# Optimization experiments

Hardware: AMD Instinct MI355X
Metric: run time of the kernel (lower is better)

The kernel has to match this reference:

```python
import jax, jax.numpy as jnp
import numpy as np

T = 2048      # sequence length (block_size)
C = 4096      # n_embd
H = 32        # n_head
KVH = 8       # n_kv_head
D = 128       # head_dim = n_embd // n_head
NEG_INF = -40000.0
ROPE_BASE = 10000.0


def setup_inputs() -> dict:
    key = jax.random.key(0)
    ks = jax.random.split(key, 5)
    x = jax.random.normal(ks[0], (T, C), jnp.float32)
    # nn.Linear weights stored as (in, out); y = x @ W. Small init for numerical sanity.
    Wq = jax.random.normal(ks[1], (C, H * D), jnp.float32) * 0.02
    Wk = jax.random.normal(ks[2], (C, KVH * D), jnp.float32) * 0.02
    Wv = jax.random.normal(ks[3], (C, KVH * D), jnp.float32) * 0.02
    Wo = jax.random.normal(ks[4], (C, C), jnp.float32) * 0.02
    # Standard LLaMA-style RoPE tables: (T, D)
    inv_freq = 1.0 / (ROPE_BASE ** (np.arange(0, D, 2, dtype=np.float32) / D))
    freqs = np.outer(np.arange(T, dtype=np.float32), inv_freq)  # (T, D/2)
    emb = np.concatenate([freqs, freqs], axis=-1)                # (T, D)
    cos = jnp.asarray(np.cos(emb), jnp.float32)
    sin = jnp.asarray(np.sin(emb), jnp.float32)
    # Additive causal mask (T, T): 0 on/below diagonal, neg_inf above.
    causal = np.tril(np.ones((T, T), dtype=bool))
    mask = jnp.where(jnp.asarray(causal), 0.0, NEG_INF).astype(jnp.float32)
    return {"x": x, "Wq": Wq, "Wk": Wk, "Wv": Wv, "Wo": Wo,
            "cos": cos, "sin": sin, "mask": mask}


def _rotate_half(u):
    u1, u2 = jnp.split(u, 2, axis=-1)
    return jnp.concatenate([-u2, u1], axis=-1)


def _apply_rope(u, cos, sin):
    # u: (heads, T, D); cos/sin: (T, D) broadcast over heads
    return u * cos + _rotate_half(u) * sin


def reference(x, Wq, Wk, Wv, Wo, cos, sin, mask):
    Tn = x.shape[0]
    q = (x @ Wq).reshape(Tn, H, D).transpose(1, 0, 2)      # (H, T, D)
    k = (x @ Wk).reshape(Tn, KVH, D).transpose(1, 0, 2)    # (KVH, T, D)
    v = (x @ Wv).reshape(Tn, KVH, D).transpose(1, 0, 2)    # (KVH, T, D)
    q = _apply_rope(q, cos, sin)
    k = _apply_rope(k, cos, sin)
    out_k, out_v = k, v
    # GQA expand: each kv head repeated contiguously H//KVH times
    rep = H // KVH
    ke = jnp.repeat(k, rep, axis=0)                         # (H, T, D)
    ve = jnp.repeat(v, rep, axis=0)                         # (H, T, D)
    # NOTE: no 1/sqrt(D) scaling in the original module
    att = jnp.einsum('htd,hsd->hts', q, ke) + mask          # (H, T, T)
    att = jax.nn.softmax(att, axis=-1)
    y = jnp.einsum('hts,hsd->htd', att, ve)                 # (H, T, D)
    y = y.transpose(1, 0, 2).reshape(Tn, C) @ Wo            # (T, C)
    return (y, out_k, out_v)
```

## Files before the change

kernel.cpp:

```cpp
#include <hip/hip_runtime.h>
#include <hip/hip_bf16.h>

#define T 2048
#define C 4096
#define H 32
#define KVH 8
#define D 128

typedef __bf16 bf16x8 __attribute__((ext_vector_type(8)));
typedef __bf16 bf16x4 __attribute__((ext_vector_type(4)));
typedef float floatx4 __attribute__((ext_vector_type(4)));

#define MFMA16 __builtin_amdgcn_mfma_f32_16x16x32_bf16

template <int NTERMS>
__device__ __forceinline__ void gemm_split_body(
    const float* __restrict__ A, const float* __restrict__ B,
    float* __restrict__ Cm, int N, int K, int row0, int col0) {
  __shared__ __bf16 Ah[128][40], Al[128][40], Bh[128][40];
  __shared__ __bf16 Bl[NTERMS == 3 ? 128 : 1][NTERMS == 3 ? 40 : 1];
  const int tid = threadIdx.x;
  const int lane = tid & 63;
  const int w = tid >> 6;
  const int n16 = lane & 15;
  const int quad = lane >> 4;
  const int wm = w >> 1, wn = w & 1;

  floatx4 acc[4][4];
#pragma unroll
  for (int mi = 0; mi < 4; ++mi)
#pragma unroll
    for (int ni = 0; ni < 4; ++ni) acc[mi][ni] = (floatx4){0.f, 0.f, 0.f, 0.f};

  const int ar = tid >> 3;
  const int ak = (tid & 7) * 4;
  const int bg = tid >> 7;
  const int bn = tid & 127;

  for (int k0 = 0; k0 < K; k0 += 32) {
#pragma unroll
    for (int p = 0; p < 4; ++p) {
      const int r = p * 32 + ar;
      const float4 av = *(const float4*)(A + (size_t)(row0 + r) * K + k0 + ak);
      bf16x4 h, l;
      h[0] = (__bf16)av.x; l[0] = (__bf16)(av.x - (float)h[0]);
      h[1] = (__bf16)av.y; l[1] = (__bf16)(av.y - (float)h[1]);
      h[2] = (__bf16)av.z; l[2] = (__bf16)(av.z - (float)h[2]);
      h[3] = (__bf16)av.w; l[3] = (__bf16)(av.w - (float)h[3]);
      *(bf16x4*)(&Ah[r][ak]) = h;
      *(bf16x4*)(&Al[r][ak]) = l;
    }
#pragma unroll
    for (int p = 0; p < 4; ++p) {
      const int kb = bg * 16 + p * 4;
      const float* bp = B + (size_t)(k0 + kb) * N + col0 + bn;
      const float f0 = bp[0];
      const float f1 = bp[(size_t)N];
      const float f2 = bp[(size_t)2 * N];
      const float f3 = bp[(size_t)3 * N];
      bf16x4 h;
      h[0] = (__bf16)f0;
      h[1] = (__bf16)f1;
      h[2] = (__bf16)f2;
      h[3] = (__bf16)f3;
      *(bf16x4*)(&Bh[bn][kb]) = h;
      if constexpr (NTERMS == 3) {
        bf16x4 l;
        l[0] = (__bf16)(f0 - (float)h[0]);
        l[1] = (__bf16)(f1 - (float)h[1]);
        l[2] = (__bf16)(f2 - (float)h[2]);
        l[3] = (__bf16)(f3 - (float)h[3]);
        *(bf16x4*)(&Bl[bn][kb]) = l;
      }
    }
    __syncthreads();
    bf16x8 a_h[4], a_l[4], b_h[4], b_l[4];
#pragma unroll
    for (int mi = 0; mi < 4; ++mi) {
      a_h[mi] = *(const bf16x8*)(&Ah[wm * 64 + mi * 16 + n16][quad * 8]);
      a_l[mi] = *(const bf16x8*)(&Al[wm * 64 + mi * 16 + n16][quad * 8]);
    }
#pragma unroll
    for (int ni = 0; ni < 4; ++ni) {
      b_h[ni] = *(const bf16x8*)(&Bh[wn * 64 + ni * 16 + n16][quad * 8]);
      if constexpr (NTERMS == 3)
        b_l[ni] = *(const bf16x8*)(&Bl[wn * 64 + ni * 16 + n16][quad * 8]);
    }
#pragma unroll
    for (int mi = 0; mi < 4; ++mi)
#pragma unroll
      for (int ni = 0; ni < 4; ++ni) {
        acc[mi][ni] = MFMA16(a_h[mi], b_h[ni], acc[mi][ni], 0, 0, 0);
        acc[mi][ni] = MFMA16(a_l[mi], b_h[ni], acc[mi][ni], 0, 0, 0);
        if constexpr (NTERMS == 3)
          acc[mi][ni] = MFMA16(a_h[mi], b_l[ni], acc[mi][ni], 0, 0, 0);
      }
    __syncthreads();
  }
#pragma unroll
  for (int mi = 0; mi < 4; ++mi)
#pragma unroll
    for (int i = 0; i < 4; ++i) {
      const int r = row0 + wm * 64 + mi * 16 + quad * 4 + i;
      float* cp = Cm + (size_t)r * N + col0 + wn * 64 + n16;
#pragma unroll
      for (int ni = 0; ni < 4; ++ni) cp[ni * 16] = acc[mi][ni][i];
    }
}

template <int NTERMS>
__global__ __launch_bounds__(256) void gemm_split_t(
    const float* __restrict__ A, const float* __restrict__ B,
    float* __restrict__ Cm, int N, int K) {
  gemm_split_body<NTERMS>(A, B, Cm, N, K, blockIdx.y * 128, blockIdx.x * 128);
}

__global__ __launch_bounds__(256) void gemm_qkv(
    const float* __restrict__ x, const float* __restrict__ Wq,
    const float* __restrict__ Wk, const float* __restrict__ Wv,
    float* __restrict__ q_ws, float* __restrict__ k_ws,
    float* __restrict__ v_ws) {
  const int bx = blockIdx.x;
  const int row0 = blockIdx.y * 128;
  if (bx < 32) {
    gemm_split_body<3>(x, Wq, q_ws, H * D, C, row0, bx * 128);
  } else if (bx < 40) {
    gemm_split_body<3>(x, Wk, k_ws, KVH * D, C, row0, (bx - 32) * 128);
  } else {
    gemm_split_body<2>(x, Wv, v_ws, KVH * D, C, row0, (bx - 40) * 128);
  }
}

__global__ __launch_bounds__(256) void convert_k(
    const float* __restrict__ k_ws, float* __restrict__ out_k,
    __bf16* __restrict__ khi, __bf16* __restrict__ klo,
    const float* __restrict__ cosb, const float* __restrict__ sinb) {
  int idx = blockIdx.x * 256 + threadIdx.x;
  if (idx >= KVH * T * 64) return;
  int d = idx & 63;
  int t = (idx >> 6) & (T - 1);
  int kvh = idx >> 17;
  const float* kp = k_ws + (size_t)t * (KVH * D) + kvh * D;
  float u1 = kp[d];
  float u2 = kp[d + 64];
  float cv = cosb[(size_t)t * D + d];
  float sv = sinb[(size_t)t * D + d];
  float r1 = u1 * cv - u2 * sv;
  float r2 = u2 * cv + u1 * sv;
  size_t base = ((size_t)kvh * T + t) * D + d;
  out_k[base] = r1;
  out_k[base + 64] = r2;
  __bf16 h1 = (__bf16)r1;
  khi[base] = h1;
  klo[base] = (__bf16)(r1 - (float)h1);
  __bf16 h2 = (__bf16)r2;
  khi[base + 64] = h2;
  klo[base + 64] = (__bf16)(r2 - (float)h2);
}

__global__ __launch_bounds__(256) void convert_v(
    const float* __restrict__ v_ws, float* __restrict__ out_v,
    __bf16* __restrict__ vt) {
  __shared__ __bf16 tile[64][65];
  const int t0 = blockIdx.x * 64;
  const int d0 = blockIdx.y * 64;
  const int kvh = blockIdx.z;
#pragma unroll
  for (int p = 0; p < 16; ++p) {
    int i = p * 256 + threadIdx.x;
    int r = i >> 6;
    int c = i & 63;
    float f = v_ws[(size_t)(t0 + r) * (KVH * D) + kvh * D + d0 + c];
    out_v[((size_t)kvh * T + t0 + r) * D + d0 + c] = f;
    tile[r][c] = (__bf16)f;
  }
  __syncthreads();
#pragma unroll
  for (int p = 0; p < 16; ++p) {
    int i = p * 256 + threadIdx.x;
    int dd = i >> 6;
    int tt = i & 63;
    vt[((size_t)kvh * D + d0 + dd) * T + t0 + tt] = tile[tt][dd];
  }
}

struct StageRegs { bf16x8 k0, k1, l0, l1, v0, v1; };

__device__ __forceinline__ void stage_load(
    StageRegs& s, const __bf16* __restrict__ Kh, const __bf16* __restrict__ Kl,
    const __bf16* __restrict__ Vt, int j0, int tid) {
  const int kr = tid >> 4, kj = (tid & 15) * 8;
  s.k0 = *(const bf16x8*)(Kh + (size_t)(j0 + kr) * D + kj);
  s.k1 = *(const bf16x8*)(Kh + (size_t)(j0 + kr + 16) * D + kj);
  s.l0 = *(const bf16x8*)(Kl + (size_t)(j0 + kr) * D + kj);
  s.l1 = *(const bf16x8*)(Kl + (size_t)(j0 + kr + 16) * D + kj);
  const int vd = tid >> 2, vj = (tid & 3) * 8;
  s.v0 = *(const bf16x8*)(Vt + (size_t)vd * T + j0 + vj);
  s.v1 = *(const bf16x8*)(Vt + (size_t)(vd + 64) * T + j0 + vj);
}

__device__ __forceinline__ void stage_write(
    const StageRegs& s, __bf16* __restrict__ KhL, __bf16* __restrict__ KlL,
    __bf16* __restrict__ VL, int tid) {
  const int kr = tid >> 4, kj = (tid & 15) * 8;
  *(bf16x8*)(KhL + kr * 136 + kj) = s.k0;
  *(bf16x8*)(KhL + (kr + 16) * 136 + kj) = s.k1;
  *(bf16x8*)(KlL + kr * 136 + kj) = s.l0;
  *(bf16x8*)(KlL + (kr + 16) * 136 + kj) = s.l1;
  const int vd = tid >> 2, vj = (tid & 3) * 8;
  *(bf16x8*)(VL + vd * 40 + vj) = s.v0;
  *(bf16x8*)(VL + (vd + 64) * 40 + vj) = s.v1;
}

__device__ __forceinline__ void load_q_rope(
    const float* __restrict__ qr, const float* __restrict__ cosb,
    const float* __restrict__ sinb, int trow, int quad,
    bf16x8* __restrict__ qh, bf16x8* __restrict__ ql) {
  float u[4][8];
#pragma unroll
  for (int c = 0; c < 4; ++c) {
    *(float4*)&u[c][0] = *(const float4*)(qr + c * 32 + quad * 8);
    *(float4*)&u[c][4] = *(const float4*)(qr + c * 32 + quad * 8 + 4);
  }
  float cv[2][8], sv[2][8];
#pragma unroll
  for (int c = 0; c < 2; ++c) {
    const float* cp = cosb + (size_t)trow * D + c * 32 + quad * 8;
    const float* sp = sinb + (size_t)trow * D + c * 32 + quad * 8;
    *(float4*)&cv[c][0] = *(const float4*)cp;
    *(float4*)&cv[c][4] = *(const float4*)(cp + 4);
    *(float4*)&sv[c][0] = *(const float4*)sp;
    *(float4*)&sv[c][4] = *(const float4*)(sp + 4);
  }
#pragma unroll
  for (int c = 0; c < 4; ++c) {
    const int cc = c & 1;
#pragma unroll
    for (int jj = 0; jj < 8; ++jj) {
      float r = (c < 2) ? (u[c][jj] * cv[cc][jj] - u[c + 2][jj] * sv[cc][jj])
                        : (u[c][jj] * cv[cc][jj] + u[c - 2][jj] * sv[cc][jj]);
      __bf16 hi = (__bf16)r;
      qh[c][jj] = hi;
      ql[c][jj] = (__bf16)(r - (float)hi);
    }
  }
}

__device__ __forceinline__ void softmax_pv(
    floatx4 s0, floatx4 s1,
    const __bf16* __restrict__ VT, __bf16* __restrict__ Pw,
    floatx4* __restrict__ O, float* __restrict__ m_i, float* __restrict__ l_i,
    int j0, int r_base, int n16, int quad) {
  if (j0 + 31 > r_base) {
#pragma unroll
    for (int i = 0; i < 4; ++i) {
      int r = r_base + quad * 4 + i;
      if (j0 + n16 > r) s0[i] = -INFINITY;
      if (j0 + 16 + n16 > r) s1[i] = -INFINITY;
    }
  }
  float p0[4], p1[4];
#pragma unroll
  for (int i = 0; i < 4; ++i) {
    float mt = fmaxf(s0[i], s1[i]);
    mt = fmaxf(mt, __shfl_xor(mt, 1));
    mt = fmaxf(mt, __shfl_xor(mt, 2));
    mt = fmaxf(mt, __shfl_xor(mt, 4));
    mt = fmaxf(mt, __shfl_xor(mt, 8));
    float mn = fmaxf(m_i[i], mt);
    float alpha = __expf(m_i[i] - mn);
    m_i[i] = mn;
    p0[i] = __expf(s0[i] - mn);
    p1[i] = __expf(s1[i] - mn);
    float rs = p0[i] + p1[i];
    rs += __shfl_xor(rs, 1);
    rs += __shfl_xor(rs, 2);
    rs += __shfl_xor(rs, 4);
    rs += __shfl_xor(rs, 8);
    l_i[i] = l_i[i] * alpha + rs;
#pragma unroll
    for (int dt = 0; dt < 8; ++dt) O[dt][i] *= alpha;
  }
#pragma unroll
  for (int i = 0; i < 4; ++i) {
    Pw[(quad * 4 + i) * 40 + n16] = (__bf16)p0[i];
    Pw[(quad * 4 + i) * 40 + n16 + 16] = (__bf16)p1[i];
  }
  bf16x8 pA = *(const bf16x8*)(Pw + n16 * 40 + quad * 8);
#pragma unroll
  for (int dt = 0; dt < 8; ++dt) {
    bf16x8 vB = *(const bf16x8*)(VT + (dt * 16 + n16) * 40 + quad * 8);
    O[dt] = MFMA16(pA, vB, O[dt], 0, 0, 0);
  }
}

template <bool BOTH>
__device__ __forceinline__ void attn_tile2(
    const __bf16* __restrict__ KhT, const __bf16* __restrict__ KlT,
    const __bf16* __restrict__ VT, __bf16* __restrict__ Pw,
    const bf16x8* qh_hi, const bf16x8* ql_hi,
    const bf16x8* qh_lo, const bf16x8* ql_lo,
    floatx4* O_hi, float* m_hi, float* l_hi,
    floatx4* O_lo, float* m_lo, float* l_lo,
    int j0, int rb_hi, int rb_lo, int n16, int quad) {
  floatx4 sh0 = {0.f, 0.f, 0.f, 0.f}, sh1 = {0.f, 0.f, 0.f, 0.f};
  floatx4 sl0 = {0.f, 0.f, 0.f, 0.f}, sl1 = {0.f, 0.f, 0.f, 0.f};
#pragma unroll
  for (int c = 0; c < 4; ++c) {
    const int off = c * 32 + quad * 8;
    bf16x8 k0h = *(const bf16x8*)(KhT + n16 * 136 + off);
    bf16x8 k1h = *(const bf16x8*)(KhT + (n16 + 16) * 136 + off);
    bf16x8 k0l = *(const bf16x8*)(KlT + n16 * 136 + off);
    bf16x8 k1l = *(const bf16x8*)(KlT + (n16 + 16) * 136 + off);
    sh0 = MFMA16(qh_hi[c], k0h, sh0, 0, 0, 0);
    sh0 = MFMA16(ql_hi[c], k0h, sh0, 0, 0, 0);
    sh0 = MFMA16(qh_hi[c], k0l, sh0, 0, 0, 0);
    sh1 = MFMA16(qh_hi[c], k1h, sh1, 0, 0, 0);
    sh1 = MFMA16(ql_hi[c], k1h, sh1, 0, 0, 0);
    sh1 = MFMA16(qh_hi[c], k1l, sh1, 0, 0, 0);
    if (BOTH) {
      sl0 = MFMA16(qh_lo[c], k0h, sl0, 0, 0, 0);
      sl0 = MFMA16(ql_lo[c], k0h, sl0, 0, 0, 0);
      sl0 = MFMA16(qh_lo[c], k0l, sl0, 0, 0, 0);
      sl1 = MFMA16(qh_lo[c], k1h, sl1, 0, 0, 0);
      sl1 = MFMA16(ql_lo[c], k1h, sl1, 0, 0, 0);
      sl1 = MFMA16(qh_lo[c], k1l, sl1, 0, 0, 0);
    }
  }
  softmax_pv(sh0, sh1, VT, Pw, O_hi, m_hi, l_hi, j0, rb_hi, n16, quad);
  if (BOTH) softmax_pv(sl0, sl1, VT, Pw, O_lo, m_lo, l_lo, j0, rb_lo, n16, quad);
}

__global__ __launch_bounds__(256, 2) void flash_attn(
    float* __restrict__ q,
    const __bf16* __restrict__ khi,
    const __bf16* __restrict__ klo,
    const __bf16* __restrict__ vt,
    const float* __restrict__ cosb,
    const float* __restrict__ sinb) {
  __shared__ __attribute__((aligned(16))) __bf16 KhL[2][32 * 136];
  __shared__ __attribute__((aligned(16))) __bf16 KlL[2][32 * 136];
  __shared__ __attribute__((aligned(16))) __bf16 VL[2][128 * 40];
  __shared__ __attribute__((aligned(16))) __bf16 Pst[4][16 * 40];

  const int tid = threadIdx.x;
  const int w = tid >> 6;
  const int lane = tid & 63;
  const int n16 = lane & 15;
  const int quad = lane >> 4;
  const int h = blockIdx.y;
  const int kvh = h >> 2;
  const int p_lo = blockIdx.x;
  const int p_hi = 31 - p_lo;
  const int rb_lo = p_lo * 64 + w * 16;
  const int rb_hi = p_hi * 64 + w * 16;
  const int nt = 64 - 2 * p_lo;
  const int nt_lo = (rb_lo + 15) / 32 + 1;
  const int nt_hi = (rb_hi + 15) / 32 + 1;

  const __bf16* Kh = khi + (size_t)kvh * T * D;
  const __bf16* Kl = klo + (size_t)kvh * T * D;
  const __bf16* Vt = vt + (size_t)kvh * D * T;

  bf16x8 qh_lo[4], ql_lo[4], qh_hi[4], ql_hi[4];
  load_q_rope(q + (size_t)(rb_lo + n16) * C + h * D, cosb, sinb,
              rb_lo + n16, quad, qh_lo, ql_lo);
  load_q_rope(q + (size_t)(rb_hi + n16) * C + h * D, cosb, sinb,
              rb_hi + n16, quad, qh_hi, ql_hi);

  floatx4 O_lo[8], O_hi[8];
#pragma unroll
  for (int dt = 0; dt < 8; ++dt) {
    O_lo[dt] = (floatx4){0.f, 0.f, 0.f, 0.f};
    O_hi[dt] = (floatx4){0.f, 0.f, 0.f, 0.f};
  }
  float m_lo[4] = {-INFINITY, -INFINITY, -INFINITY, -INFINITY};
  float m_hi[4] = {-INFINITY, -INFINITY, -INFINITY, -INFINITY};
  float l_lo[4] = {0.f, 0.f, 0.f, 0.f};
  float l_hi[4] = {0.f, 0.f, 0.f, 0.f};

  StageRegs sreg;
  stage_load(sreg, Kh, Kl, Vt, 0, tid);
  stage_write(sreg, KhL[0], KlL[0], VL[0], tid);
  __syncthreads();

  __bf16* Pw = Pst[w];
  for (int t = 0; t < nt; ++t) {
    const int cur = t & 1;
    const int j0 = t * 32;
    if (t + 1 < nt) stage_load(sreg, Kh, Kl, Vt, j0 + 32, tid);
    if (t < nt_hi) {
      if (t < nt_lo)
        attn_tile2<true>(KhL[cur], KlL[cur], VL[cur], Pw,
                         qh_hi, ql_hi, qh_lo, ql_lo,
                         O_hi, m_hi, l_hi, O_lo, m_lo, l_lo,
                         j0, rb_hi, rb_lo, n16, quad);
      else
        attn_tile2<false>(KhL[cur], KlL[cur], VL[cur], Pw,
                          qh_hi, ql_hi, qh_lo, ql_lo,
                          O_hi, m_hi, l_hi, O_lo, m_lo, l_lo,
                          j0, rb_hi, rb_lo, n16, quad);
    }
    if (t + 1 < nt) stage_write(sreg, KhL[cur ^ 1], KlL[cur ^ 1], VL[cur ^ 1], tid);
    __syncthreads();
  }

#pragma unroll
  for (int i = 0; i < 4; ++i) {
    float inv_l = 1.0f / l_lo[i];
    float inv_h = 1.0f / l_hi[i];
    int r_l = rb_lo + quad * 4 + i;
    int r_h = rb_hi + quad * 4 + i;
    float* yl = q + (size_t)r_l * C + h * D + n16;
    float* yh = q + (size_t)r_h * C + h * D + n16;
#pragma unroll
    for (int dt = 0; dt < 8; ++dt) {
      yl[dt * 16] = O_lo[dt][i] * inv_l;
      yh[dt * 16] = O_hi[dt][i] * inv_h;
    }
  }
}

extern "C" void kernel_launch(void* const* d_in, const int* in_sizes, int n_in,
                              void* d_out, int out_size, void* d_ws, size_t ws_size,
                              hipStream_t stream) {
  (void)in_sizes; (void)n_in; (void)out_size; (void)ws_size;
  const float* x    = (const float*)d_in[0];
  const float* Wq   = (const float*)d_in[1];
  const float* Wk   = (const float*)d_in[2];
  const float* Wv   = (const float*)d_in[3];
  const float* Wo   = (const float*)d_in[4];
  const float* cosb = (const float*)d_in[5];
  const float* sinb = (const float*)d_in[6];

  float* q_ws = (float*)d_ws;
  float* k_ws = q_ws + (size_t)T * C;
  float* v_ws = k_ws + (size_t)T * KVH * D;
  __bf16* khi = (__bf16*)(v_ws + (size_t)T * KVH * D);
  __bf16* klo = khi + (size_t)KVH * T * D;
  __bf16* vt  = klo + (size_t)KVH * T * D;

  float* out_y = (float*)d_out;
  float* out_k = out_y + (size_t)T * C;
  float* out_v = out_k + (size_t)KVH * T * D;

  dim3 blk(256);
  gemm_qkv<<<dim3(48, T / 128), blk, 0, stream>>>(x, Wq, Wk, Wv, q_ws, k_ws, v_ws);
  convert_k<<<(KVH * T * 64 + 255) / 256, blk, 0, stream>>>(k_ws, out_k, khi, klo, cosb, sinb);
  convert_v<<<dim3(T / 64, D / 64, KVH), blk, 0, stream>>>(v_ws, out_v, vt);
  flash_attn<<<dim3(16, H), blk, 0, stream>>>(q_ws, khi, klo, vt, cosb, sinb);
  gemm_split_t<2><<<dim3(C / 128, T / 128), blk, 0, stream>>>(q_ws, Wo, out_y, C, C);
}
```

Baseline: 904.0 us.

## Fuse K RoPE and V transpose epilogues into the QKV projection GEMM

The QKV GEMM now writes its outputs directly in final form. For K it applies RoPE and emits the fp32 output plus bf16 hi/lo splits. For V it emits the fp32 output and a transposed bf16 copy through shared memory. Column ownership per wave is remapped so each thread holds both the d and d+64 elements needed for rotation. This removes two separate conversion kernels and the fp32 workspace round trip for K and V. The cost is that V now also uses the three-term split, which adds a small amount of extra MFMA work.

```diff
diff --git a/kernel.cpp b/kernel.cpp
--- a/kernel.cpp
+++ b/kernel.cpp
@@ -13,35 +13,33 @@
 
 #define MFMA16 __builtin_amdgcn_mfma_f32_16x16x32_bf16
 
-template <int NTERMS>
-__device__ __forceinline__ void gemm_split_body(
+__device__ __forceinline__ void qkv_compute3(
     const float* __restrict__ A, const float* __restrict__ B,
-    float* __restrict__ Cm, int N, int K, int row0, int col0) {
-  __shared__ __bf16 Ah[128][40], Al[128][40], Bh[128][40];
-  __shared__ __bf16 Bl[NTERMS == 3 ? 128 : 1][NTERMS == 3 ? 40 : 1];
+    int N, int row0, int col0,
+    __bf16 (&Ah)[128][40], __bf16 (&Al)[128][40],
+    __bf16 (&Bh)[128][40], __bf16 (&Bl)[128][40],
+    floatx4 (&acc)[4][4]) {
   const int tid = threadIdx.x;
   const int lane = tid & 63;
   const int w = tid >> 6;
   const int n16 = lane & 15;
   const int quad = lane >> 4;
   const int wm = w >> 1, wn = w & 1;
-
-  floatx4 acc[4][4];
-#pragma unroll
-  for (int mi = 0; mi < 4; ++mi)
-#pragma unroll
-    for (int ni = 0; ni < 4; ++ni) acc[mi][ni] = (floatx4){0.f, 0.f, 0.f, 0.f};
-
   const int ar = tid >> 3;
   const int ak = (tid & 7) * 4;
   const int bg = tid >> 7;
   const int bn = tid & 127;
 
-  for (int k0 = 0; k0 < K; k0 += 32) {
+  int bcol[4];
+#pragma unroll
+  for (int ni = 0; ni < 4; ++ni)
+    bcol[ni] = wn * 32 + (ni & 1) * 16 + (ni >> 1) * 64 + n16;
+
+  for (int k0 = 0; k0 < C; k0 += 32) {
 #pragma unroll
     for (int p = 0; p < 4; ++p) {
       const int r = p * 32 + ar;
-      const float4 av = *(const float4*)(A + (size_t)(row0 + r) * K + k0 + ak);
+      const float4 av = *(const float4*)(A + (size_t)(row0 + r) * C + k0 + ak);
       bf16x4 h, l;
       h[0] = (__bf16)av.x; l[0] = (__bf16)(av.x - (float)h[0]);
       h[1] = (__bf16)av.y; l[1] = (__bf16)(av.y - (float)h[1]);
@@ -58,20 +56,13 @@
       const float f1 = bp[(size_t)N];
       const float f2 = bp[(size_t)2 * N];
       const float f3 = bp[(size_t)3 * N];
-      bf16x4 h;
-      h[0] = (__bf16)f0;
-      h[1] = (__bf16)f1;
-      h[2] = (__bf16)f2;
-      h[3] = (__bf16)f3;
+      bf16x4 h, l;
+      h[0] = (__bf16)f0; l[0] = (__bf16)(f0 - (float)h[0]);
+      h[1] = (__bf16)f1; l[1] = (__bf16)(f1 - (float)h[1]);
+      h[2] = (__bf16)f2; l[2] = (__bf16)(f2 - (float)h[2]);
+      h[3] = (__bf16)f3; l[3] = (__bf16)(f3 - (float)h[3]);
       *(bf16x4*)(&Bh[bn][kb]) = h;
-      if constexpr (NTERMS == 3) {
-        bf16x4 l;
-        l[0] = (__bf16)(f0 - (float)h[0]);
-        l[1] = (__bf16)(f1 - (float)h[1]);
-        l[2] = (__bf16)(f2 - (float)h[2]);
-        l[3] = (__bf16)(f3 - (float)h[3]);
-        *(bf16x4*)(&Bl[bn][kb]) = l;
-      }
+      *(bf16x4*)(&Bl[bn][kb]) = l;
     }
     __syncthreads();
     bf16x8 a_h[4], a_l[4], b_h[4], b_l[4];
@@ -82,9 +73,8 @@
     }
 #pragma unroll
     for (int ni = 0; ni < 4; ++ni) {
-      b_h[ni] = *(const bf16x8*)(&Bh[wn * 64 + ni * 16 + n16][quad * 8]);
-      if constexpr (NTERMS == 3)
-        b_l[ni] = *(const bf16x8*)(&Bl[wn * 64 + ni * 16 + n16][quad * 8]);
+      b_h[ni] = *(const bf16x8*)(&Bh[bcol[ni]][quad * 8]);
+      b_l[ni] = *(const bf16x8*)(&Bl[bcol[ni]][quad * 8]);
     }
 #pragma unroll
     for (int mi = 0; mi < 4; ++mi)
@@ -92,8 +82,183 @@
       for (int ni = 0; ni < 4; ++ni) {
         acc[mi][ni] = MFMA16(a_h[mi], b_h[ni], acc[mi][ni], 0, 0, 0);
         acc[mi][ni] = MFMA16(a_l[mi], b_h[ni], acc[mi][ni], 0, 0, 0);
-        if constexpr (NTERMS == 3)
-          acc[mi][ni] = MFMA16(a_h[mi], b_l[ni], acc[mi][ni], 0, 0, 0);
+        acc[mi][ni] = MFMA16(a_h[mi], b_l[ni], acc[mi][ni], 0, 0, 0);
+      }
+    __syncthreads();
+  }
+}
+
+__global__ __launch_bounds__(256) void gemm_qkv(
+    const float* __restrict__ x, const float* __restrict__ Wq,
+    const float* __restrict__ Wk, const float* __restrict__ Wv,
+    float* __restrict__ q_ws, float* __restrict__ out_k,
+    __bf16* __restrict__ khi, __bf16* __restrict__ klo,
+    float* __restrict__ out_v, __bf16* __restrict__ vt,
+    const float* __restrict__ cosb, const float* __restrict__ sinb) {
+  __shared__ __bf16 Ah[128][40], Al[128][40], Bh[128][40], Bl[128][40];
+  const int bx = blockIdx.x;
+  const int row0 = blockIdx.y * 128;
+  const float* B;
+  int N, col0, mode;
+  if (bx < 32)      { B = Wq; N = H * D;   col0 = bx * 128;        mode = 0; }
+  else if (bx < 40) { B = Wk; N = KVH * D; col0 = (bx - 32) * 128; mode = 1; }
+  else              { B = Wv; N = KVH * D; col0 = (bx - 40) * 128; mode = 2; }
+
+  floatx4 acc[4][4];
+#pragma unroll
+  for (int mi = 0; mi < 4; ++mi)
+#pragma unroll
+    for (int ni = 0; ni < 4; ++ni) acc[mi][ni] = (floatx4){0.f, 0.f, 0.f, 0.f};
+
+  qkv_compute3(x, B, N, row0, col0, Ah, Al, Bh, Bl, acc);
+
+  const int lane = threadIdx.x & 63;
+  const int w = threadIdx.x >> 6;
+  const int n16 = lane & 15;
+  const int quad = lane >> 4;
+  const int wm = w >> 1, wn = w & 1;
+  int bcol[4];
+#pragma unroll
+  for (int ni = 0; ni < 4; ++ni)
+    bcol[ni] = wn * 32 + (ni & 1) * 16 + (ni >> 1) * 64 + n16;
+
+  if (mode == 0) {
+#pragma unroll
+    for (int mi = 0; mi < 4; ++mi)
+#pragma unroll
+      for (int i = 0; i < 4; ++i) {
+        const int r = row0 + wm * 64 + mi * 16 + quad * 4 + i;
+        float* cp = q_ws + (size_t)r * (H * D) + col0;
+#pragma unroll
+        for (int ni = 0; ni < 4; ++ni) cp[bcol[ni]] = acc[mi][ni][i];
+      }
+  } else if (mode == 1) {
+    const int kvh = col0 >> 7;
+#pragma unroll
+    for (int mi = 0; mi < 4; ++mi)
+#pragma unroll
+      for (int i = 0; i < 4; ++i) {
+        const int t = row0 + wm * 64 + mi * 16 + quad * 4 + i;
+#pragma unroll
+        for (int ni = 0; ni < 2; ++ni) {
+          const int dlo = bcol[ni];
+          const float cv = cosb[(size_t)t * D + dlo];
+          const float sv = sinb[(size_t)t * D + dlo];
+          const float a = acc[mi][ni][i];
+          const float b = acc[mi][ni + 2][i];
+          const float r1 = a * cv - b * sv;
+          const float r2 = b * cv + a * sv;
+          const size_t base = ((size_t)kvh * T + t) * D + dlo;
+          out_k[base] = r1;
+          out_k[base + 64] = r2;
+          const __bf16 h1 = (__bf16)r1;
+          khi[base] = h1;
+          klo[base] = (__bf16)(r1 - (float)h1);
+          const __bf16 h2 = (__bf16)r2;
+          khi[base + 64] = h2;
+          klo[base + 64] = (__bf16)(r2 - (float)h2);
+        }
+      }
+  } else {
+    const int kvh = col0 >> 7;
+#pragma unroll
+    for (int mi = 0; mi < 4; ++mi)
+#pragma unroll
+      for (int i = 0; i < 4; ++i) {
+        const int r = row0 + wm * 64 + mi * 16 + quad * 4 + i;
+        float* cp = out_v + ((size_t)kvh * T + r) * D;
+#pragma unroll
+        for (int ni = 0; ni < 4; ++ni) cp[bcol[ni]] = acc[mi][ni][i];
+      }
+    __bf16 (*tile)[129] = (__bf16(*)[129])(&Ah[0][0]);
+#pragma unroll
+    for (int mi = 0; mi < 4; ++mi)
+#pragma unroll
+      for (int i = 0; i < 4; ++i) {
+        const int tl = wm * 64 + mi * 16 + quad * 4 + i;
+#pragma unroll
+        for (int ni = 0; ni < 4; ++ni)
+          tile[tl][bcol[ni]] = (__bf16)acc[mi][ni][i];
+      }
+    __syncthreads();
+#pragma unroll
+    for (int p = 0; p < 8; ++p) {
+      const int idx = p * 256 + threadIdx.x;
+      const int d = idx >> 4;
+      const int t0l = (idx & 15) * 8;
+      bf16x8 v8;
+#pragma unroll
+      for (int j = 0; j < 8; ++j) v8[j] = tile[t0l + j][d];
+      *(bf16x8*)(vt + ((size_t)kvh * D + d) * T + row0 + t0l) = v8;
+    }
+  }
+}
+
+__global__ __launch_bounds__(256) void gemm_wo(
+    const float* __restrict__ A, const float* __restrict__ B,
+    float* __restrict__ Cm) {
+  __shared__ __bf16 Ah[128][40], Al[128][40], Bh[128][40];
+  const int N = C;
+  const int row0 = blockIdx.y * 128;
+  const int col0 = blockIdx.x * 128;
+  const int tid = threadIdx.x;
+  const int lane = tid & 63;
+  const int w = tid >> 6;
+  const int n16 = lane & 15;
+  const int quad = lane >> 4;
+  const int wm = w >> 1, wn = w & 1;
+
+  floatx4 acc[4][4];
+#pragma unroll
+  for (int mi = 0; mi < 4; ++mi)
+#pragma unroll
+    for (int ni = 0; ni < 4; ++ni) acc[mi][ni] = (floatx4){0.f, 0.f, 0.f, 0.f};
+
+  const int ar = tid >> 3;
+  const int ak = (tid & 7) * 4;
+  const int bg = tid >> 7;
+  const int bn = tid & 127;
+
+  for (int k0 = 0; k0 < C; k0 += 32) {
+#pragma unroll
+    for (int p = 0; p < 4; ++p) {
+      const int r = p * 32 + ar;
+      const float4 av = *(const float4*)(A + (size_t)(row0 + r) * C + k0 + ak);
+      bf16x4 h, l;
+      h[0] = (__bf16)av.x; l[0] = (__bf16)(av.x - (float)h[0]);
+      h[1] = (__bf16)av.y; l[1] = (__bf16)(av.y - (float)h[1]);
+      h[2] = (__bf16)av.z; l[2] = (__bf16)(av.z - (float)h[2]);
+      h[3] = (__bf16)av.w; l[3] = (__bf16)(av.w - (float)h[3]);
+      *(bf16x4*)(&Ah[r][ak]) = h;
+      *(bf16x4*)(&Al[r][ak]) = l;
+    }
+#pragma unroll
+    for (int p = 0; p < 4; ++p) {
+      const int kb = bg * 16 + p * 4;
+      const float* bp = B + (size_t)(k0 + kb) * N + col0 + bn;
+      bf16x4 h;
+      h[0] = (__bf16)bp[0];
+      h[1] = (__bf16)bp[(size_t)N];
+      h[2] = (__bf16)bp[(size_t)2 * N];
+      h[3] = (__bf16)bp[(size_t)3 * N];
+      *(bf16x4*)(&Bh[bn][kb]) = h;
+    }
+    __syncthreads();
+    bf16x8 a_h[4], a_l[4], b_h[4];
+#pragma unroll
+    for (int mi = 0; mi < 4; ++mi) {
+      a_h[mi] = *(const bf16x8*)(&Ah[wm * 64 + mi * 16 + n16][quad * 8]);
+      a_l[mi] = *(const bf16x8*)(&Al[wm * 64 + mi * 16 + n16][quad * 8]);
+    }
+#pragma unroll
+    for (int ni = 0; ni < 4; ++ni)
+      b_h[ni] = *(const bf16x8*)(&Bh[wn * 64 + ni * 16 + n16][quad * 8]);
+#pragma unroll
+    for (int mi = 0; mi < 4; ++mi)
+#pragma unroll
+      for (int ni = 0; ni < 4; ++ni) {
+        acc[mi][ni] = MFMA16(a_h[mi], b_h[ni], acc[mi][ni], 0, 0, 0);
+        acc[mi][ni] = MFMA16(a_l[mi], b_h[ni], acc[mi][ni], 0, 0, 0);
       }
     __syncthreads();
   }
@@ -106,82 +271,6 @@
 #pragma unroll
       for (int ni = 0; ni < 4; ++ni) cp[ni * 16] = acc[mi][ni][i];
     }
-}
-
-template <int NTERMS>
-__global__ __launch_bounds__(256) void gemm_split_t(
-    const float* __restrict__ A, const float* __restrict__ B,
-    float* __restrict__ Cm, int N, int K) {
-  gemm_split_body<NTERMS>(A, B, Cm, N, K, blockIdx.y * 128, blockIdx.x * 128);
-}
-
-__global__ __launch_bounds__(256) void gemm_qkv(
-    const float* __restrict__ x, const float* __restrict__ Wq,
-    const float* __restrict__ Wk, const float* __restrict__ Wv,
-    float* __restrict__ q_ws, float* __restrict__ k_ws,
-    float* __restrict__ v_ws) {
-  const int bx = blockIdx.x;
-  const int row0 = blockIdx.y * 128;
-  if (bx < 32) {
-    gemm_split_body<3>(x, Wq, q_ws, H * D, C, row0, bx * 128);
-  } else if (bx < 40) {
-    gemm_split_body<3>(x, Wk, k_ws, KVH * D, C, row0, (bx - 32) * 128);
-  } else {
-    gemm_split_body<2>(x, Wv, v_ws, KVH * D, C, row0, (bx - 40) * 128);
-  }
-}
-
-__global__ __launch_bounds__(256) void convert_k(
-    const float* __restrict__ k_ws, float* __restrict__ out_k,
-    __bf16* __restrict__ khi, __bf16* __restrict__ klo,
-    const float* __restrict__ cosb, const float* __restrict__ sinb) {
-  int idx = blockIdx.x * 256 + threadIdx.x;
-  if (idx >= KVH * T * 64) return;
-  int d = idx & 63;
-  int t = (idx >> 6) & (T - 1);
-  int kvh = idx >> 17;
-  const float* kp = k_ws + (size_t)t * (KVH * D) + kvh * D;
-  float u1 = kp[d];
-  float u2 = kp[d + 64];
-  float cv = cosb[(size_t)t * D + d];
-  float sv = sinb[(size_t)t * D + d];
-  float r1 = u1 * cv - u2 * sv;
-  float r2 = u2 * cv + u1 * sv;
-  size_t base = ((size_t)kvh * T + t) * D + d;
-  out_k[base] = r1;
-  out_k[base + 64] = r2;
-  __bf16 h1 = (__bf16)r1;
-  khi[base] = h1;
-  klo[base] = (__bf16)(r1 - (float)h1);
-  __bf16 h2 = (__bf16)r2;
-  khi[base + 64] = h2;
-  klo[base + 64] = (__bf16)(r2 - (float)h2);
-}
-
-__global__ __launch_bounds__(256) void convert_v(
-    const float* __restrict__ v_ws, float* __restrict__ out_v,
-    __bf16* __restrict__ vt) {
-  __shared__ __bf16 tile[64][65];
-  const int t0 = blockIdx.x * 64;
-  const int d0 = blockIdx.y * 64;
-  const int kvh = blockIdx.z;
-#pragma unroll
-  for (int p = 0; p < 16; ++p) {
-    int i = p * 256 + threadIdx.x;
-    int r = i >> 6;
-    int c = i & 63;
-    float f = v_ws[(size_t)(t0 + r) * (KVH * D) + kvh * D + d0 + c];
-    out_v[((size_t)kvh * T + t0 + r) * D + d0 + c] = f;
-    tile[r][c] = (__bf16)f;
-  }
-  __syncthreads();
-#pragma unroll
-  for (int p = 0; p < 16; ++p) {
-    int i = p * 256 + threadIdx.x;
-    int dd = i >> 6;
-    int tt = i & 63;
-    vt[((size_t)kvh * D + d0 + dd) * T + t0 + tt] = tile[tt][dd];
-  }
 }
 
 struct StageRegs { bf16x8 k0, k1, l0, l1, v0, v1; };
@@ -434,9 +523,7 @@
   const float* sinb = (const float*)d_in[6];
 
   float* q_ws = (float*)d_ws;
-  float* k_ws = q_ws + (size_t)T * C;
-  float* v_ws = k_ws + (size_t)T * KVH * D;
-  __bf16* khi = (__bf16*)(v_ws + (size_t)T * KVH * D);
+  __bf16* khi = (__bf16*)(q_ws + (size_t)T * C);
   __bf16* klo = khi + (size_t)KVH * T * D;
   __bf16* vt  = klo + (size_t)KVH * T * D;
 
@@ -445,9 +532,8 @@
   float* out_v = out_k + (size_t)KVH * T * D;
 
   dim3 blk(256);
-  gemm_qkv<<<dim3(48, T / 128), blk, 0, stream>>>(x, Wq, Wk, Wv, q_ws, k_ws, v_ws);
-  convert_k<<<(KVH * T * 64 + 255) / 256, blk, 0, stream>>>(k_ws, out_k, khi, klo, cosb, sinb);
-  convert_v<<<dim3(T / 64, D / 64, KVH), blk, 0, stream>>>(v_ws, out_v, vt);
+  gemm_qkv<<<dim3(48, T / 128), blk, 0, stream>>>(
+      x, Wq, Wk, Wv, q_ws, out_k, khi, klo, out_v, vt, cosb, sinb);
   flash_attn<<<dim3(16, H), blk, 0, stream>>>(q_ws, khi, klo, vt, cosb, sinb);
-  gemm_split_t<2><<<dim3(C / 128, T / 128), blk, 0, stream>>>(q_ws, Wo, out_y, C, C);
-}
+  gemm_wo<<<dim3(C / 128, T / 128), blk, 0, stream>>>(q_ws, Wo, out_y);
+}
```

New measurement: 947.3 us. +4.8%, slower.
